# Kernel tuning notes

Measured on AMD Instinct MI355X. Metric: run time of the kernel, lower is better.

The kernel has to match this reference:

```python
import jax, jax.numpy as jnp
import numpy as np

NUM_HEADS = 16
HEAD_DIM = 64
ROPE_BASE = 160000.0


def _rope_tables(seq_len, head_dim):
    inv_freq = 1.0 / (ROPE_BASE ** (jnp.arange(0, head_dim, 2, dtype=jnp.float32) / head_dim))
    freqs = jnp.arange(seq_len, dtype=jnp.float32)[:, None] * inv_freq[None, :]  # [S, hd/2]
    return jnp.cos(freqs)[None, None], jnp.sin(freqs)[None, None]  # [1,1,S,hd/2]


def _apply_rope(x, cos, sin):
    # x: [B, nh, S, hd]; split-half rotation as in the torch module
    x1, x2 = jnp.split(x, 2, axis=-1)
    return jnp.concatenate([x1 * cos - x2 * sin, x2 * cos + x1 * sin], axis=-1)


def setup_inputs() -> dict:
    key = jax.random.key(0)
    k1, k2, k3 = jax.random.split(key, 3)
    B, S, H = 2, 2048, 1024
    hidden_states = jax.random.normal(k1, (B, S, H), dtype=jnp.float32)
    # additive causal mask: 0 for allowed, -1e9 for future positions
    causal = jnp.tril(jnp.ones((S, S), dtype=bool))
    attention_mask = jnp.where(causal, 0.0, -1e9).astype(jnp.float32)[None, None]
    Wqkv = jax.random.normal(k2, (H, 3 * H), dtype=jnp.float32) * (H ** -0.5)
    Wo = jax.random.normal(k3, (H, H), dtype=jnp.float32) * (H ** -0.5)
    return {"hidden_states": hidden_states, "attention_mask": attention_mask, "Wqkv": Wqkv, "Wo": Wo}


def reference(hidden_states, attention_mask, Wqkv, Wo):
    B, S, H = hidden_states.shape
    nh, hd = NUM_HEADS, HEAD_DIM
    scale = hd ** -0.5

    qkv = hidden_states @ Wqkv                                   # [B,S,3H]
    qkv = qkv.reshape(B, S, 3, nh, hd).transpose(2, 0, 3, 1, 4)  # [3,B,nh,S,hd]
    q, k, v = qkv[0], qkv[1], qkv[2]

    cos, sin = _rope_tables(S, hd)
    q = _apply_rope(q, cos, sin)
    k = _apply_rope(k, cos, sin)

    scores = jnp.einsum('bhqd,bhkd->bhqk', q, k) * scale + attention_mask
    attn = jax.nn.softmax(scores, axis=-1)
    out = jnp.einsum('bhqk,bhkd->bhqd', attn, v)                 # [B,nh,S,hd]
    out = out.transpose(0, 2, 1, 3).reshape(B, S, H)
    return out @ Wo
```

## Files before the change

### kernel.cpp

```cpp
#include <hip/hip_runtime.h>
#include <hip/hip_bf16.h>

typedef __bf16 bf16x8 __attribute__((ext_vector_type(8)));
typedef float f32x4 __attribute__((ext_vector_type(4)));
typedef unsigned short u16;

__device__ __forceinline__ u16 f2bf(float f) {
    union { float f; unsigned u; } x{f};
    unsigned r = x.u + 0x7fffu + ((x.u >> 16) & 1u);
    return (u16)(r >> 16);
}
__device__ __forceinline__ unsigned pk2(float a, float b) {
    union { float f; unsigned u; } x{a}, y{b};
    return ((x.u + 0x8000u) >> 16) | ((y.u + 0x8000u) & 0xffff0000u);
}
__device__ __forceinline__ float ex2(float x) { return __builtin_amdgcn_exp2f(x); }
__device__ __forceinline__ f32x4 zero4() { f32x4 z = {0.f, 0.f, 0.f, 0.f}; return z; }

__global__ void __launch_bounds__(256) prep(const float* __restrict__ hs,
                                            u16* __restrict__ Xb,
                                            const float* __restrict__ Wqkv,
                                            u16* __restrict__ Wqkvt,
                                            const float* __restrict__ Wo,
                                            u16* __restrict__ Wot,
                                            float* __restrict__ cosT,
                                            float* __restrict__ sinT) {
    __shared__ float tile[32][33];
    const int blk = blockIdx.x, t = threadIdx.x;
    if (blk < 4096) {
        int i = (blk * 256 + t) * 4;
        float4 v = *(const float4*)(hs + i);
        ushort4 o;
        o.x = f2bf(v.x); o.y = f2bf(v.y); o.z = f2bf(v.z); o.w = f2bf(v.w);
        *(ushort4*)(Xb + i) = o;
    } else if (blk < 8192) {
        const float* W; u16* Wt; int N, bx, by;
        if (blk < 7168) { int bid = blk - 4096; W = Wqkv; Wt = Wqkvt; N = 3072; bx = bid % 96; by = bid / 96; }
        else            { int bid = blk - 7168; W = Wo;   Wt = Wot;   N = 1024; bx = bid % 32; by = bid / 32; }
        const int K = 1024;
        int tx = t & 31, ty = t >> 5;
        int n0 = bx * 32, k0 = by * 32;
#pragma unroll
        for (int i = 0; i < 32; i += 8)
            tile[ty + i][tx] = W[(size_t)(k0 + ty + i) * N + n0 + tx];
        __syncthreads();
#pragma unroll
        for (int i = 0; i < 32; i += 8)
            Wt[(size_t)(n0 + ty + i) * K + k0 + tx] = f2bf(tile[tx][ty + i]);
    } else {
        int idx = (blk - 8192) * 256 + t;
        int d = idx & 31, s = idx >> 5;
        float inv = expf(-(float)d * 0.374466538f);
        float th = (float)s * inv;
        cosT[idx] = cosf(th);
        sinT[idx] = sinf(th);
    }
}

struct GemmCtx {
    f32x4 acc[4][4];
    int m16, q4, wm, wn;
};
template <int KDIM>
__device__ __forceinline__ void gemm_loop(const u16* __restrict__ A,
                                          const u16* __restrict__ Bt,
                                          int bm, int bn, GemmCtx& cx,
                                          u16 (*As)[128][40], u16 (*Bs)[128][40]) {
    const int t = threadIdx.x;
    const int lane = t & 63, w = t >> 6;
    cx.wm = w >> 1; cx.wn = w & 1;
    cx.m16 = lane & 15; cx.q4 = lane >> 4;
    const int r = t >> 1, c0 = (t & 1) * 16;

    const u16* Ag = A + (size_t)(bm * 128 + r) * KDIM + c0;
    const u16* Bg = Bt + (size_t)(bn * 128 + r) * KDIM + c0;

#pragma unroll
    for (int i = 0; i < 4; i++)
#pragma unroll
        for (int j = 0; j < 4; j++) cx.acc[i][j] = zero4();

    uint4 a0 = *(const uint4*)(Ag);
    uint4 a1 = *(const uint4*)(Ag + 8);
    uint4 b0 = *(const uint4*)(Bg);
    uint4 b1 = *(const uint4*)(Bg + 8);

    for (int k0 = 0; k0 < KDIM; k0 += 32) {
        const int bi = (k0 >> 5) & 1;
        *(uint4*)&As[bi][r][c0] = a0; *(uint4*)&As[bi][r][c0 + 8] = a1;
        *(uint4*)&Bs[bi][r][c0] = b0; *(uint4*)&Bs[bi][r][c0 + 8] = b1;
        if (k0 + 32 < KDIM) {
            a0 = *(const uint4*)(Ag + k0 + 32);
            a1 = *(const uint4*)(Ag + k0 + 40);
            b0 = *(const uint4*)(Bg + k0 + 32);
            b1 = *(const uint4*)(Bg + k0 + 40);
        }
        __syncthreads();
        bf16x8 af[4], bf[4];
#pragma unroll
        for (int i = 0; i < 4; i++)
            af[i] = *(const bf16x8*)&As[bi][cx.wm * 64 + i * 16 + cx.m16][cx.q4 * 8];
#pragma unroll
        for (int j = 0; j < 4; j++)
            bf[j] = *(const bf16x8*)&Bs[bi][cx.wn * 64 + j * 16 + cx.m16][cx.q4 * 8];
#pragma unroll
        for (int i = 0; i < 4; i++)
#pragma unroll
            for (int j = 0; j < 4; j++)
                cx.acc[i][j] = __builtin_amdgcn_mfma_f32_16x16x32_bf16(af[i], bf[j], cx.acc[i][j], 0, 0, 0);
    }
}

__global__ void __launch_bounds__(256) gemm_qkv(const u16* __restrict__ A,
                                                const u16* __restrict__ Bt,
                                                const float* __restrict__ cosT,
                                                const float* __restrict__ sinT,
                                                u16* __restrict__ Q,
                                                u16* __restrict__ Kd,
                                                u16* __restrict__ Vt) {
    __shared__ __align__(16) u16 As[2][128][40];
    __shared__ __align__(16) u16 Bs[2][128][40];
    GemmCtx cx;
    const int bm = blockIdx.y, bn = blockIdx.x;
    gemm_loop<1024>(A, Bt, bm, bn, cx, As, Bs);
    const int m16 = cx.m16, q4 = cx.q4;

    const int colbase = bn * 128 + cx.wn * 64;
    const int type = colbase >> 10;
    const int h = (colbase & 1023) >> 6;
    const int rbase = bm * 128 + cx.wm * 64;

    if (type == 2) {
#pragma unroll
        for (int i = 0; i < 4; i++) {
            int s0 = rbase + i * 16 + q4 * 4;
            int b = s0 >> 11, sl = s0 & 2047;
            size_t ob = (size_t)(b * 16 + h) * 64 * 2048;
#pragma unroll
            for (int j = 0; j < 4; j++) {
                int d = j * 16 + m16;
                ushort4 o;
                o.x = f2bf(cx.acc[i][j][0]);
                o.y = f2bf(cx.acc[i][j][1]);
                o.z = f2bf(cx.acc[i][j][2]);
                o.w = f2bf(cx.acc[i][j][3]);
                *(ushort4*)&Vt[ob + (size_t)d * 2048 + sl] = o;
            }
        }
    } else {
        u16* dst = (type == 0) ? Q : Kd;
        const float qs = (type == 0) ? 0.1803368801f  : 1.0f;
#pragma unroll
        for (int i = 0; i < 4; i++)
#pragma unroll
            for (int rr = 0; rr < 4; rr++) {
                int r = rbase + i * 16 + q4 * 4 + rr;
                int b = r >> 11, s = r & 2047;
                size_t ob = ((size_t)((b * 16 + h) * 2048 + s)) * 64;
#pragma unroll
                for (int j2 = 0; j2 < 2; j2++) {
                    int d = j2 * 16 + m16;
                    float cs = cosT[s * 32 + d];
                    float sn = sinT[s * 32 + d];
                    float x1 = cx.acc[i][j2][rr];
                    float x2 = cx.acc[i][j2 + 2][rr];
                    dst[ob + d]      = f2bf((x1 * cs - x2 * sn) * qs);
                    dst[ob + d + 32] = f2bf((x2 * cs + x1 * sn) * qs);
                }
            }
    }
}

__global__ void __launch_bounds__(256) gemm_out(const u16* __restrict__ A,
                                                const u16* __restrict__ Bt,
                                                float* __restrict__ C) {
    __shared__ __align__(16) u16 As[2][128][40];
    __shared__ __align__(16) u16 Bs[2][128][40];
    GemmCtx cx;
    const int bm = blockIdx.y, bn = blockIdx.x;
    gemm_loop<1024>(A, Bt, bm, bn, cx, As, Bs);
    const int N = 1024;
#pragma unroll
    for (int i = 0; i < 4; i++)
#pragma unroll
        for (int j = 0; j < 4; j++)
#pragma unroll
            for (int rr = 0; rr < 4; rr++) {
                int row = bm * 128 + cx.wm * 64 + i * 16 + cx.q4 * 4 + rr;
                int col = bn * 128 + cx.wn * 64 + j * 16 + cx.m16;
                C[(size_t)row * N + col] = cx.acc[i][j][rr];
            }
}

__global__ void __launch_bounds__(256) attn_kernel(const u16* __restrict__ Q,
                                                   const u16* __restrict__ Kg_,
                                                   const u16* __restrict__ Vtg_,
                                                   u16* __restrict__ O) {
    __shared__ __align__(16) u16 Ks[2][64][72];
    __shared__ __align__(16) u16 Vt[2][64][72];
    __shared__ __align__(16) u16 Pt[4][16][72];
    const int t = threadIdx.x, w = t >> 6;
    const int m16 = t & 15, q4 = (t & 63) >> 4;
    const int bx = blockIdx.x, bh = blockIdx.y;
    const size_t base = (size_t)bh * 2048 * 64;
    const int b = bh >> 4, h = bh & 15;
    const int skey = t >> 2, sc = (t & 3) * 16;

#pragma unroll 1
    for (int ph = 0; ph < 2; ph++) {
        const int qt = ph ? (31 - bx) : bx;
        const int qrow = qt * 64 + w * 16 + m16;
        const u16* Qg = Q + base + (size_t)qrow * 64;
        bf16x8 qf0 = *(const bf16x8*)(Qg + q4 * 8);
        bf16x8 qf1 = *(const bf16x8*)(Qg + 32 + q4 * 8);

        f32x4 occ[4];
#pragma unroll
        for (int dc = 0; dc < 4; dc++) occ[dc] = zero4();
        float li = 0.f;

        const u16* Kb0 = Kg_ + base + skey * 64 + sc;
        const u16* Vt0 = Vtg_ + base + (size_t)skey * 2048 + sc;
        uint4 ka = *(const uint4*)(Kb0);
        uint4 kb = *(const uint4*)(Kb0 + 8);
        uint4 va = *(const uint4*)(Vt0);
        uint4 vb = *(const uint4*)(Vt0 + 8);

#pragma unroll 1
        for (int jt = 0; jt <= qt; jt++) {
            const int bi = jt & 1;
            *(uint4*)&Ks[bi][skey][sc] = ka;
            *(uint4*)&Ks[bi][skey][sc + 8] = kb;
            *(uint4*)&Vt[bi][skey][sc] = va;
            *(uint4*)&Vt[bi][skey][sc + 8] = vb;
            if (jt < qt) {
                const u16* Kn = Kb0 + (size_t)(jt + 1) * 4096;
                const u16* Vn = Vt0 + (size_t)(jt + 1) * 64;
                ka = *(const uint4*)(Kn);
                kb = *(const uint4*)(Kn + 8);
                va = *(const uint4*)(Vn);
                vb = *(const uint4*)(Vn + 8);
            }
            __syncthreads();

            f32x4 st[4];
#pragma unroll
            for (int c = 0; c < 4; c++) st[c] = zero4();
#pragma unroll
            for (int c = 0; c < 4; c++) {
                bf16x8 kf0 = *(const bf16x8*)&Ks[bi][c * 16 + m16][q4 * 8];
                bf16x8 kf1 = *(const bf16x8*)&Ks[bi][c * 16 + m16][32 + q4 * 8];
                st[c] = __builtin_amdgcn_mfma_f32_16x16x32_bf16(kf0, qf0, st[c], 0, 0, 0);
                st[c] = __builtin_amdgcn_mfma_f32_16x16x32_bf16(kf1, qf1, st[c], 0, 0, 0);
            }

            float pv[4][4];
#pragma unroll
            for (int c = 0; c < 4; c++)
#pragma unroll
                for (int rr = 0; rr < 4; rr++) pv[c][rr] = st[c][rr];
            if (jt == qt) {
                const int ql = w * 16 + m16;
#pragma unroll
                for (int c = 0; c < 4; c++)
#pragma unroll
                    for (int rr = 0; rr < 4; rr++)
                        if (c * 16 + q4 * 4 + rr > ql) pv[c][rr] = -1e30f;
            }

#pragma unroll
            for (int c = 0; c < 4; c++) {
                float p0 = ex2(pv[c][0] - 24.f);
                float p1 = ex2(pv[c][1] - 24.f);
                float p2 = ex2(pv[c][2] - 24.f);
                float p3 = ex2(pv[c][3] - 24.f);
                li += (p0 + p1) + (p2 + p3);
                uint2 pkd = make_uint2(pk2(p0, p1), pk2(p2, p3));
                *(uint2*)&Pt[w][m16][c * 16 + q4 * 4] = pkd;
            }

#pragma unroll
            for (int ks = 0; ks < 2; ks++) {
                bf16x8 pf = *(const bf16x8*)&Pt[w][m16][ks * 32 + q4 * 8];
#pragma unroll
                for (int dc = 0; dc < 4; dc++) {
                    bf16x8 vf = *(const bf16x8*)&Vt[bi][dc * 16 + m16][ks * 32 + q4 * 8];
                    occ[dc] = __builtin_amdgcn_mfma_f32_16x16x32_bf16(vf, pf, occ[dc], 0, 0, 0);
                }
            }
        }

        li += __shfl_xor(li, 16);
        li += __shfl_xor(li, 32);
        float rli = 1.0f / li;
        u16* Op = O + ((size_t)(b * 2048 + qrow)) * 1024 + h * 64 + q4 * 4;
#pragma unroll
        for (int dc = 0; dc < 4; dc++) {
            ushort4 o;
            o.x = f2bf(occ[dc][0] * rli);
            o.y = f2bf(occ[dc][1] * rli);
            o.z = f2bf(occ[dc][2] * rli);
            o.w = f2bf(occ[dc][3] * rli);
            *(ushort4*)(Op + dc * 16) = o;
        }
        __syncthreads();
    }
}

extern "C" void kernel_launch(void* const* d_in, const int* in_sizes, int n_in,
                              void* d_out, int out_size, void* d_ws, size_t ws_size,
                              hipStream_t stream) {
    const float* hs   = (const float*)d_in[0];
    const float* Wqkv = (const float*)d_in[2];
    const float* Wo   = (const float*)d_in[3];
    float* out = (float*)d_out;

    const int BS = 4096;
    const int H = 1024, N3 = 3072;
    const int SH = 32 * 2048 * 64;

    u16* Xb    = (u16*)d_ws;
    u16* Wqkvt = Xb + (size_t)BS * H;
    u16* Wot   = Wqkvt + (size_t)N3 * H;
    u16* Qb    = Wot + (size_t)H * H;
    u16* Kb    = Qb + SH;
    u16* Vtb   = Kb + SH;
    u16* AOb   = Vtb + SH;
    float* cosT = (float*)(AOb + (size_t)BS * H);
    float* sinT = cosT + 2048 * 32;

    prep<<<8448, 256, 0, stream>>>(hs, Xb, Wqkv, Wqkvt, Wo, Wot, cosT, sinT);

    gemm_qkv<<<dim3(N3 / 128, BS / 128), 256, 0, stream>>>(Xb, Wqkvt, cosT, sinT,
                                                           Qb, Kb, Vtb);

    attn_kernel<<<dim3(16, 32), 256, 0, stream>>>(Qb, Kb, Vtb, AOb);

    gemm_out<<<dim3(H / 128, BS / 128), 256, 0, stream>>>(AOb, Wot, out);
}
```

Baseline: 201.1 us.

## Load GEMM A operand straight to registers; attention handles two query tiles per block

In the shared GEMM loop, each wave now loads its A fragments directly from global memory into registers, prefetched one k-step ahead. Only B is staged through shared memory, and the k loop is fully unrolled. This removes the A LDS writes and reads but doubles global reads of A, since both column-waves fetch the same rows. The attention kernel drops the balanced pairing of query tiles bx and 31-bx. Each block now processes two adjacent 64-row query tiles that share every K/V tile load from LDS, which halves K/V staging per query row but makes work per block uneven across the grid.

```diff
diff --git a/kernel.cpp b/kernel.cpp
--- a/kernel.cpp
+++ b/kernel.cpp
@@ -65,41 +65,45 @@
 __device__ __forceinline__ void gemm_loop(const u16* __restrict__ A,
                                           const u16* __restrict__ Bt,
                                           int bm, int bn, GemmCtx& cx,
-                                          u16 (*As)[128][40], u16 (*Bs)[128][40]) {
+                                          u16 (*Bs)[128][40]) {
     const int t = threadIdx.x;
     const int lane = t & 63, w = t >> 6;
     cx.wm = w >> 1; cx.wn = w & 1;
     cx.m16 = lane & 15; cx.q4 = lane >> 4;
     const int r = t >> 1, c0 = (t & 1) * 16;
 
-    const u16* Ag = A + (size_t)(bm * 128 + r) * KDIM + c0;
     const u16* Bg = Bt + (size_t)(bn * 128 + r) * KDIM + c0;
+    const u16* Ag = A + (size_t)(bm * 128 + cx.wm * 64 + cx.m16) * KDIM + cx.q4 * 8;
 
 #pragma unroll
     for (int i = 0; i < 4; i++)
 #pragma unroll
         for (int j = 0; j < 4; j++) cx.acc[i][j] = zero4();
 
-    uint4 a0 = *(const uint4*)(Ag);
-    uint4 a1 = *(const uint4*)(Ag + 8);
     uint4 b0 = *(const uint4*)(Bg);
     uint4 b1 = *(const uint4*)(Bg + 8);
-
+    bf16x8 afn[4];
+#pragma unroll
+    for (int i = 0; i < 4; i++)
+        afn[i] = *(const bf16x8*)(Ag + (size_t)i * 16 * KDIM);
+
+#pragma unroll
     for (int k0 = 0; k0 < KDIM; k0 += 32) {
         const int bi = (k0 >> 5) & 1;
-        *(uint4*)&As[bi][r][c0] = a0; *(uint4*)&As[bi][r][c0 + 8] = a1;
-        *(uint4*)&Bs[bi][r][c0] = b0; *(uint4*)&Bs[bi][r][c0 + 8] = b1;
+        *(uint4*)&Bs[bi][r][c0] = b0;
+        *(uint4*)&Bs[bi][r][c0 + 8] = b1;
+        bf16x8 af[4];
+#pragma unroll
+        for (int i = 0; i < 4; i++) af[i] = afn[i];
         if (k0 + 32 < KDIM) {
-            a0 = *(const uint4*)(Ag + k0 + 32);
-            a1 = *(const uint4*)(Ag + k0 + 40);
             b0 = *(const uint4*)(Bg + k0 + 32);
             b1 = *(const uint4*)(Bg + k0 + 40);
+#pragma unroll
+            for (int i = 0; i < 4; i++)
+                afn[i] = *(const bf16x8*)(Ag + k0 + 32 + (size_t)i * 16 * KDIM);
         }
         __syncthreads();
-        bf16x8 af[4], bf[4];
-#pragma unroll
-        for (int i = 0; i < 4; i++)
-            af[i] = *(const bf16x8*)&As[bi][cx.wm * 64 + i * 16 + cx.m16][cx.q4 * 8];
+        bf16x8 bf[4];
 #pragma unroll
         for (int j = 0; j < 4; j++)
             bf[j] = *(const bf16x8*)&Bs[bi][cx.wn * 64 + j * 16 + cx.m16][cx.q4 * 8];
@@ -118,11 +122,10 @@
                                                 u16* __restrict__ Q,
                                                 u16* __restrict__ Kd,
                                                 u16* __restrict__ Vt) {
-    __shared__ __align__(16) u16 As[2][128][40];
     __shared__ __align__(16) u16 Bs[2][128][40];
     GemmCtx cx;
     const int bm = blockIdx.y, bn = blockIdx.x;
-    gemm_loop<1024>(A, Bt, bm, bn, cx, As, Bs);
+    gemm_loop<1024>(A, Bt, bm, bn, cx, Bs);
     const int m16 = cx.m16, q4 = cx.q4;
 
     const int colbase = bn * 128 + cx.wn * 64;
@@ -174,11 +177,10 @@
 __global__ void __launch_bounds__(256) gemm_out(const u16* __restrict__ A,
                                                 const u16* __restrict__ Bt,
                                                 float* __restrict__ C) {
-    __shared__ __align__(16) u16 As[2][128][40];
     __shared__ __align__(16) u16 Bs[2][128][40];
     GemmCtx cx;
     const int bm = blockIdx.y, bn = blockIdx.x;
-    gemm_loop<1024>(A, Bt, bm, bn, cx, As, Bs);
+    gemm_loop<1024>(A, Bt, bm, bn, cx, Bs);
     const int N = 1024;
 #pragma unroll
     for (int i = 0; i < 4; i++)
@@ -198,7 +200,7 @@
                                                    u16* __restrict__ O) {
     __shared__ __align__(16) u16 Ks[2][64][72];
     __shared__ __align__(16) u16 Vt[2][64][72];
-    __shared__ __align__(16) u16 Pt[4][16][72];
+    __shared__ __align__(16) u16 Pt[4][2][16][72];
     const int t = threadIdx.x, w = t >> 6;
     const int m16 = t & 15, q4 = (t & 63) >> 4;
     const int bx = blockIdx.x, bh = blockIdx.y;
@@ -206,60 +208,69 @@
     const int b = bh >> 4, h = bh & 15;
     const int skey = t >> 2, sc = (t & 3) * 16;
 
+    const int jg0 = 2 * bx;
+    const int jtmax = 2 * bx + 1;
+
+    const int qrow0 = bx * 128 + w * 16 + m16;
+    const u16* Qg = Q + base + (size_t)qrow0 * 64;
+    bf16x8 qa0 = *(const bf16x8*)(Qg + q4 * 8);
+    bf16x8 qa1 = *(const bf16x8*)(Qg + 32 + q4 * 8);
+    bf16x8 qb0 = *(const bf16x8*)(Qg + 64 * 64 + q4 * 8);
+    bf16x8 qb1 = *(const bf16x8*)(Qg + 64 * 64 + 32 + q4 * 8);
+
+    f32x4 occ0[4], occ1[4];
+#pragma unroll
+    for (int dc = 0; dc < 4; dc++) { occ0[dc] = zero4(); occ1[dc] = zero4(); }
+    float li0 = 0.f, li1 = 0.f;
+
+    const u16* Kb0 = Kg_ + base + skey * 64 + sc;
+    const u16* Vt0 = Vtg_ + base + (size_t)skey * 2048 + sc;
+    uint4 ka = *(const uint4*)(Kb0);
+    uint4 kb = *(const uint4*)(Kb0 + 8);
+    uint4 va = *(const uint4*)(Vt0);
+    uint4 vb = *(const uint4*)(Vt0 + 8);
+
 #pragma unroll 1
-    for (int ph = 0; ph < 2; ph++) {
-        const int qt = ph ? (31 - bx) : bx;
-        const int qrow = qt * 64 + w * 16 + m16;
-        const u16* Qg = Q + base + (size_t)qrow * 64;
-        bf16x8 qf0 = *(const bf16x8*)(Qg + q4 * 8);
-        bf16x8 qf1 = *(const bf16x8*)(Qg + 32 + q4 * 8);
-
-        f32x4 occ[4];
-#pragma unroll
-        for (int dc = 0; dc < 4; dc++) occ[dc] = zero4();
-        float li = 0.f;
-
-        const u16* Kb0 = Kg_ + base + skey * 64 + sc;
-        const u16* Vt0 = Vtg_ + base + (size_t)skey * 2048 + sc;
-        uint4 ka = *(const uint4*)(Kb0);
-        uint4 kb = *(const uint4*)(Kb0 + 8);
-        uint4 va = *(const uint4*)(Vt0);
-        uint4 vb = *(const uint4*)(Vt0 + 8);
-
-#pragma unroll 1
-        for (int jt = 0; jt <= qt; jt++) {
-            const int bi = jt & 1;
-            *(uint4*)&Ks[bi][skey][sc] = ka;
-            *(uint4*)&Ks[bi][skey][sc + 8] = kb;
-            *(uint4*)&Vt[bi][skey][sc] = va;
-            *(uint4*)&Vt[bi][skey][sc + 8] = vb;
-            if (jt < qt) {
-                const u16* Kn = Kb0 + (size_t)(jt + 1) * 4096;
-                const u16* Vn = Vt0 + (size_t)(jt + 1) * 64;
-                ka = *(const uint4*)(Kn);
-                kb = *(const uint4*)(Kn + 8);
-                va = *(const uint4*)(Vn);
-                vb = *(const uint4*)(Vn + 8);
-            }
-            __syncthreads();
-
-            f32x4 st[4];
-#pragma unroll
-            for (int c = 0; c < 4; c++) st[c] = zero4();
-#pragma unroll
-            for (int c = 0; c < 4; c++) {
-                bf16x8 kf0 = *(const bf16x8*)&Ks[bi][c * 16 + m16][q4 * 8];
-                bf16x8 kf1 = *(const bf16x8*)&Ks[bi][c * 16 + m16][32 + q4 * 8];
-                st[c] = __builtin_amdgcn_mfma_f32_16x16x32_bf16(kf0, qf0, st[c], 0, 0, 0);
-                st[c] = __builtin_amdgcn_mfma_f32_16x16x32_bf16(kf1, qf1, st[c], 0, 0, 0);
-            }
-
+    for (int jt = 0; jt <= jtmax; jt++) {
+        const int bi = jt & 1;
+        *(uint4*)&Ks[bi][skey][sc] = ka;
+        *(uint4*)&Ks[bi][skey][sc + 8] = kb;
+        *(uint4*)&Vt[bi][skey][sc] = va;
+        *(uint4*)&Vt[bi][skey][sc + 8] = vb;
+        if (jt < jtmax) {
+            const u16* Kn = Kb0 + (size_t)(jt + 1) * 4096;
+            const u16* Vn = Vt0 + (size_t)(jt + 1) * 64;
+            ka = *(const uint4*)(Kn);
+            kb = *(const uint4*)(Kn + 8);
+            va = *(const uint4*)(Vn);
+            vb = *(const uint4*)(Vn + 8);
+        }
+        __syncthreads();
+
+        const bool g0act = (jt <= jg0);
+
+        f32x4 st0[4], st1[4];
+#pragma unroll
+        for (int c = 0; c < 4; c++) { st0[c] = zero4(); st1[c] = zero4(); }
+#pragma unroll
+        for (int c = 0; c < 4; c++) {
+            bf16x8 kf0 = *(const bf16x8*)&Ks[bi][c * 16 + m16][q4 * 8];
+            bf16x8 kf1 = *(const bf16x8*)&Ks[bi][c * 16 + m16][32 + q4 * 8];
+            if (g0act) {
+                st0[c] = __builtin_amdgcn_mfma_f32_16x16x32_bf16(kf0, qa0, st0[c], 0, 0, 0);
+                st0[c] = __builtin_amdgcn_mfma_f32_16x16x32_bf16(kf1, qa1, st0[c], 0, 0, 0);
+            }
+            st1[c] = __builtin_amdgcn_mfma_f32_16x16x32_bf16(kf0, qb0, st1[c], 0, 0, 0);
+            st1[c] = __builtin_amdgcn_mfma_f32_16x16x32_bf16(kf1, qb1, st1[c], 0, 0, 0);
+        }
+
+        if (g0act) {
             float pv[4][4];
 #pragma unroll
             for (int c = 0; c < 4; c++)
 #pragma unroll
-                for (int rr = 0; rr < 4; rr++) pv[c][rr] = st[c][rr];
-            if (jt == qt) {
+                for (int rr = 0; rr < 4; rr++) pv[c][rr] = st0[c][rr];
+            if (jt == jg0) {
                 const int ql = w * 16 + m16;
 #pragma unroll
                 for (int c = 0; c < 4; c++)
@@ -267,43 +278,75 @@
                     for (int rr = 0; rr < 4; rr++)
                         if (c * 16 + q4 * 4 + rr > ql) pv[c][rr] = -1e30f;
             }
-
 #pragma unroll
             for (int c = 0; c < 4; c++) {
                 float p0 = ex2(pv[c][0] - 24.f);
                 float p1 = ex2(pv[c][1] - 24.f);
                 float p2 = ex2(pv[c][2] - 24.f);
                 float p3 = ex2(pv[c][3] - 24.f);
-                li += (p0 + p1) + (p2 + p3);
-                uint2 pkd = make_uint2(pk2(p0, p1), pk2(p2, p3));
-                *(uint2*)&Pt[w][m16][c * 16 + q4 * 4] = pkd;
-            }
-
-#pragma unroll
-            for (int ks = 0; ks < 2; ks++) {
-                bf16x8 pf = *(const bf16x8*)&Pt[w][m16][ks * 32 + q4 * 8];
-#pragma unroll
-                for (int dc = 0; dc < 4; dc++) {
-                    bf16x8 vf = *(const bf16x8*)&Vt[bi][dc * 16 + m16][ks * 32 + q4 * 8];
-                    occ[dc] = __builtin_amdgcn_mfma_f32_16x16x32_bf16(vf, pf, occ[dc], 0, 0, 0);
-                }
-            }
-        }
-
-        li += __shfl_xor(li, 16);
-        li += __shfl_xor(li, 32);
-        float rli = 1.0f / li;
-        u16* Op = O + ((size_t)(b * 2048 + qrow)) * 1024 + h * 64 + q4 * 4;
-#pragma unroll
-        for (int dc = 0; dc < 4; dc++) {
-            ushort4 o;
-            o.x = f2bf(occ[dc][0] * rli);
-            o.y = f2bf(occ[dc][1] * rli);
-            o.z = f2bf(occ[dc][2] * rli);
-            o.w = f2bf(occ[dc][3] * rli);
-            *(ushort4*)(Op + dc * 16) = o;
-        }
-        __syncthreads();
+                li0 += (p0 + p1) + (p2 + p3);
+                *(uint2*)&Pt[w][0][m16][c * 16 + q4 * 4] = make_uint2(pk2(p0, p1), pk2(p2, p3));
+            }
+        }
+        {
+            float pv[4][4];
+#pragma unroll
+            for (int c = 0; c < 4; c++)
+#pragma unroll
+                for (int rr = 0; rr < 4; rr++) pv[c][rr] = st1[c][rr];
+            if (jt == jtmax) {
+                const int ql = w * 16 + m16;
+#pragma unroll
+                for (int c = 0; c < 4; c++)
+#pragma unroll
+                    for (int rr = 0; rr < 4; rr++)
+                        if (c * 16 + q4 * 4 + rr > ql) pv[c][rr] = -1e30f;
+            }
+#pragma unroll
+            for (int c = 0; c < 4; c++) {
+                float p0 = ex2(pv[c][0] - 24.f);
+                float p1 = ex2(pv[c][1] - 24.f);
+                float p2 = ex2(pv[c][2] - 24.f);
+                float p3 = ex2(pv[c][3] - 24.f);
+                li1 += (p0 + p1) + (p2 + p3);
+                *(uint2*)&Pt[w][1][m16][c * 16 + q4 * 4] = make_uint2(pk2(p0, p1), pk2(p2, p3));
+            }
+        }
+
+#pragma unroll
+        for (int ks = 0; ks < 2; ks++) {
+            bf16x8 pf0, pf1;
+            if (g0act) pf0 = *(const bf16x8*)&Pt[w][0][m16][ks * 32 + q4 * 8];
+            pf1 = *(const bf16x8*)&Pt[w][1][m16][ks * 32 + q4 * 8];
+#pragma unroll
+            for (int dc = 0; dc < 4; dc++) {
+                bf16x8 vf = *(const bf16x8*)&Vt[bi][dc * 16 + m16][ks * 32 + q4 * 8];
+                if (g0act)
+                    occ0[dc] = __builtin_amdgcn_mfma_f32_16x16x32_bf16(vf, pf0, occ0[dc], 0, 0, 0);
+                occ1[dc] = __builtin_amdgcn_mfma_f32_16x16x32_bf16(vf, pf1, occ1[dc], 0, 0, 0);
+            }
+        }
+    }
+
+    li0 += __shfl_xor(li0, 16); li0 += __shfl_xor(li0, 32);
+    li1 += __shfl_xor(li1, 16); li1 += __shfl_xor(li1, 32);
+    float r0 = 1.0f / li0, r1 = 1.0f / li1;
+    u16* Op0 = O + ((size_t)(b * 2048 + qrow0)) * 1024 + h * 64 + q4 * 4;
+    u16* Op1 = O + ((size_t)(b * 2048 + qrow0 + 64)) * 1024 + h * 64 + q4 * 4;
+#pragma unroll
+    for (int dc = 0; dc < 4; dc++) {
+        ushort4 o;
+        o.x = f2bf(occ0[dc][0] * r0);
+        o.y = f2bf(occ0[dc][1] * r0);
+        o.z = f2bf(occ0[dc][2] * r0);
+        o.w = f2bf(occ0[dc][3] * r0);
+        *(ushort4*)(Op0 + dc * 16) = o;
+        ushort4 p;
+        p.x = f2bf(occ1[dc][0] * r1);
+        p.y = f2bf(occ1[dc][1] * r1);
+        p.z = f2bf(occ1[dc][2] * r1);
+        p.w = f2bf(occ1[dc][3] * r1);
+        *(ushort4*)(Op1 + dc * 16) = p;
     }
 }
 
```

After: 243.7 us. +21.2%, slower.

## Use direct global-to-LDS loads in GEMMs and 128-row query tiles in attention

Applied to the files above, without the earlier changes.

The GEMM main loop now uses global_load_lds async copies into a single XOR-swizzled LDS buffer, replacing register-staged double buffering. This removes the VGPR round trip but adds a second barrier per k-step and loses prefetch overlap. The attention kernel moves to 512-thread blocks covering 128 query rows, so each K/V tile loaded into shared memory serves twice as many queries. The diagonal tile is handled by per-wave skipping and masking, and the launch grid is halved to 256 blocks, which may reduce occupancy.

```diff
diff --git a/kernel.cpp b/kernel.cpp
--- a/kernel.cpp
+++ b/kernel.cpp
@@ -16,6 +16,12 @@
 }
 __device__ __forceinline__ float ex2(float x) { return __builtin_amdgcn_exp2f(x); }
 __device__ __forceinline__ f32x4 zero4() { f32x4 z = {0.f, 0.f, 0.f, 0.f}; return z; }
+
+typedef const __attribute__((address_space(1))) unsigned int* gp1_t;
+typedef __attribute__((address_space(3))) unsigned int* lp3_t;
+__device__ __forceinline__ void async16(const u16* g, u16* l) {
+    __builtin_amdgcn_global_load_lds((gp1_t)g, (lp3_t)l, 16, 0, 0);
+}
 
 __global__ void __launch_bounds__(256) prep(const float* __restrict__ hs,
                                             u16* __restrict__ Xb,
@@ -65,44 +71,41 @@
 __device__ __forceinline__ void gemm_loop(const u16* __restrict__ A,
                                           const u16* __restrict__ Bt,
                                           int bm, int bn, GemmCtx& cx,
-                                          u16 (*As)[128][40], u16 (*Bs)[128][40]) {
+                                          u16* As, u16* Bs) {
     const int t = threadIdx.x;
     const int lane = t & 63, w = t >> 6;
     cx.wm = w >> 1; cx.wn = w & 1;
     cx.m16 = lane & 15; cx.q4 = lane >> 4;
-    const int r = t >> 1, c0 = (t & 1) * 16;
-
-    const u16* Ag = A + (size_t)(bm * 128 + r) * KDIM + c0;
-    const u16* Bg = Bt + (size_t)(bn * 128 + r) * KDIM + c0;
+
+    const int lrow = lane >> 2;
+    const int kchunk = (lane & 3) ^ ((lane >> 3) & 3);
+    const u16* Ag = A + (size_t)(bm * 128 + w * 32 + lrow) * KDIM + kchunk * 8;
+    const u16* Bg = Bt + (size_t)(bn * 128 + w * 32 + lrow) * KDIM + kchunk * 8;
+    u16* Al0 = As + (w * 32) * 32;
+    u16* Al1 = As + (w * 32 + 16) * 32;
+    u16* Bl0 = Bs + (w * 32) * 32;
+    u16* Bl1 = Bs + (w * 32 + 16) * 32;
+    const int kswz = (cx.q4 ^ ((cx.m16 >> 1) & 3)) * 8;
 
 #pragma unroll
     for (int i = 0; i < 4; i++)
 #pragma unroll
         for (int j = 0; j < 4; j++) cx.acc[i][j] = zero4();
 
-    uint4 a0 = *(const uint4*)(Ag);
-    uint4 a1 = *(const uint4*)(Ag + 8);
-    uint4 b0 = *(const uint4*)(Bg);
-    uint4 b1 = *(const uint4*)(Bg + 8);
-
     for (int k0 = 0; k0 < KDIM; k0 += 32) {
-        const int bi = (k0 >> 5) & 1;
-        *(uint4*)&As[bi][r][c0] = a0; *(uint4*)&As[bi][r][c0 + 8] = a1;
-        *(uint4*)&Bs[bi][r][c0] = b0; *(uint4*)&Bs[bi][r][c0 + 8] = b1;
-        if (k0 + 32 < KDIM) {
-            a0 = *(const uint4*)(Ag + k0 + 32);
-            a1 = *(const uint4*)(Ag + k0 + 40);
-            b0 = *(const uint4*)(Bg + k0 + 32);
-            b1 = *(const uint4*)(Bg + k0 + 40);
-        }
+        __syncthreads();
+        async16(Ag + k0, Al0);
+        async16(Ag + 16 * KDIM + k0, Al1);
+        async16(Bg + k0, Bl0);
+        async16(Bg + 16 * KDIM + k0, Bl1);
         __syncthreads();
         bf16x8 af[4], bf[4];
 #pragma unroll
         for (int i = 0; i < 4; i++)
-            af[i] = *(const bf16x8*)&As[bi][cx.wm * 64 + i * 16 + cx.m16][cx.q4 * 8];
+            af[i] = *(const bf16x8*)&As[(cx.wm * 64 + i * 16 + cx.m16) * 32 + kswz];
 #pragma unroll
         for (int j = 0; j < 4; j++)
-            bf[j] = *(const bf16x8*)&Bs[bi][cx.wn * 64 + j * 16 + cx.m16][cx.q4 * 8];
+            bf[j] = *(const bf16x8*)&Bs[(cx.wn * 64 + j * 16 + cx.m16) * 32 + kswz];
 #pragma unroll
         for (int i = 0; i < 4; i++)
 #pragma unroll
@@ -118,8 +121,8 @@
                                                 u16* __restrict__ Q,
                                                 u16* __restrict__ Kd,
                                                 u16* __restrict__ Vt) {
-    __shared__ __align__(16) u16 As[2][128][40];
-    __shared__ __align__(16) u16 Bs[2][128][40];
+    __shared__ __align__(16) u16 As[128 * 32];
+    __shared__ __align__(16) u16 Bs[128 * 32];
     GemmCtx cx;
     const int bm = blockIdx.y, bn = blockIdx.x;
     gemm_loop<1024>(A, Bt, bm, bn, cx, As, Bs);
@@ -174,8 +177,8 @@
 __global__ void __launch_bounds__(256) gemm_out(const u16* __restrict__ A,
                                                 const u16* __restrict__ Bt,
                                                 float* __restrict__ C) {
-    __shared__ __align__(16) u16 As[2][128][40];
-    __shared__ __align__(16) u16 Bs[2][128][40];
+    __shared__ __align__(16) u16 As[128 * 32];
+    __shared__ __align__(16) u16 Bs[128 * 32];
     GemmCtx cx;
     const int bm = blockIdx.y, bn = blockIdx.x;
     gemm_loop<1024>(A, Bt, bm, bn, cx, As, Bs);
@@ -192,24 +195,24 @@
             }
 }
 
-__global__ void __launch_bounds__(256) attn_kernel(const u16* __restrict__ Q,
+__global__ void __launch_bounds__(512) attn_kernel(const u16* __restrict__ Q,
                                                    const u16* __restrict__ Kg_,
                                                    const u16* __restrict__ Vtg_,
                                                    u16* __restrict__ O) {
     __shared__ __align__(16) u16 Ks[2][64][72];
-    __shared__ __align__(16) u16 Vt[2][64][72];
-    __shared__ __align__(16) u16 Pt[4][16][72];
+    __shared__ __align__(16) u16 Vs[2][64][72];
+    __shared__ __align__(16) u16 Pt[8][16][72];
     const int t = threadIdx.x, w = t >> 6;
     const int m16 = t & 15, q4 = (t & 63) >> 4;
     const int bx = blockIdx.x, bh = blockIdx.y;
     const size_t base = (size_t)bh * 2048 * 64;
     const int b = bh >> 4, h = bh & 15;
-    const int skey = t >> 2, sc = (t & 3) * 16;
+    const int skey = t >> 3, sc = (t & 7) * 8;
 
 #pragma unroll 1
     for (int ph = 0; ph < 2; ph++) {
-        const int qt = ph ? (31 - bx) : bx;
-        const int qrow = qt * 64 + w * 16 + m16;
+        const int st = ph ? (15 - bx) : bx;
+        const int qrow = st * 128 + w * 16 + m16;
         const u16* Qg = Q + base + (size_t)qrow * 64;
         bf16x8 qf0 = *(const bf16x8*)(Qg + q4 * 8);
         bf16x8 qf1 = *(const bf16x8*)(Qg + 32 + q4 * 8);
@@ -219,73 +222,69 @@
         for (int dc = 0; dc < 4; dc++) occ[dc] = zero4();
         float li = 0.f;
 
+        const int jtmax = 2 * st + 1;
+        const int jd = 2 * st + (w >> 2);
+
         const u16* Kb0 = Kg_ + base + skey * 64 + sc;
         const u16* Vt0 = Vtg_ + base + (size_t)skey * 2048 + sc;
         uint4 ka = *(const uint4*)(Kb0);
-        uint4 kb = *(const uint4*)(Kb0 + 8);
         uint4 va = *(const uint4*)(Vt0);
-        uint4 vb = *(const uint4*)(Vt0 + 8);
 
 #pragma unroll 1
-        for (int jt = 0; jt <= qt; jt++) {
+        for (int jt = 0; jt <= jtmax; jt++) {
             const int bi = jt & 1;
             *(uint4*)&Ks[bi][skey][sc] = ka;
-            *(uint4*)&Ks[bi][skey][sc + 8] = kb;
-            *(uint4*)&Vt[bi][skey][sc] = va;
-            *(uint4*)&Vt[bi][skey][sc + 8] = vb;
-            if (jt < qt) {
-                const u16* Kn = Kb0 + (size_t)(jt + 1) * 4096;
-                const u16* Vn = Vt0 + (size_t)(jt + 1) * 64;
-                ka = *(const uint4*)(Kn);
-                kb = *(const uint4*)(Kn + 8);
-                va = *(const uint4*)(Vn);
-                vb = *(const uint4*)(Vn + 8);
+            *(uint4*)&Vs[bi][skey][sc] = va;
+            if (jt < jtmax) {
+                ka = *(const uint4*)(Kb0 + (size_t)(jt + 1) * 4096);
+                va = *(const uint4*)(Vt0 + (size_t)(jt + 1) * 64);
             }
             __syncthreads();
 
-            f32x4 st[4];
-#pragma unroll
-            for (int c = 0; c < 4; c++) st[c] = zero4();
-#pragma unroll
-            for (int c = 0; c < 4; c++) {
-                bf16x8 kf0 = *(const bf16x8*)&Ks[bi][c * 16 + m16][q4 * 8];
-                bf16x8 kf1 = *(const bf16x8*)&Ks[bi][c * 16 + m16][32 + q4 * 8];
-                st[c] = __builtin_amdgcn_mfma_f32_16x16x32_bf16(kf0, qf0, st[c], 0, 0, 0);
-                st[c] = __builtin_amdgcn_mfma_f32_16x16x32_bf16(kf1, qf1, st[c], 0, 0, 0);
-            }
-
-            float pv[4][4];
-#pragma unroll
-            for (int c = 0; c < 4; c++)
-#pragma unroll
-                for (int rr = 0; rr < 4; rr++) pv[c][rr] = st[c][rr];
-            if (jt == qt) {
-                const int ql = w * 16 + m16;
+            if (jt <= jd) {
+                f32x4 stv[4];
+#pragma unroll
+                for (int c = 0; c < 4; c++) stv[c] = zero4();
+#pragma unroll
+                for (int c = 0; c < 4; c++) {
+                    bf16x8 kf0 = *(const bf16x8*)&Ks[bi][c * 16 + m16][q4 * 8];
+                    bf16x8 kf1 = *(const bf16x8*)&Ks[bi][c * 16 + m16][32 + q4 * 8];
+                    stv[c] = __builtin_amdgcn_mfma_f32_16x16x32_bf16(kf0, qf0, stv[c], 0, 0, 0);
+                    stv[c] = __builtin_amdgcn_mfma_f32_16x16x32_bf16(kf1, qf1, stv[c], 0, 0, 0);
+                }
+
+                float pv[4][4];
 #pragma unroll
                 for (int c = 0; c < 4; c++)
 #pragma unroll
-                    for (int rr = 0; rr < 4; rr++)
-                        if (c * 16 + q4 * 4 + rr > ql) pv[c][rr] = -1e30f;
-            }
-
-#pragma unroll
-            for (int c = 0; c < 4; c++) {
-                float p0 = ex2(pv[c][0] - 24.f);
-                float p1 = ex2(pv[c][1] - 24.f);
-                float p2 = ex2(pv[c][2] - 24.f);
-                float p3 = ex2(pv[c][3] - 24.f);
-                li += (p0 + p1) + (p2 + p3);
-                uint2 pkd = make_uint2(pk2(p0, p1), pk2(p2, p3));
-                *(uint2*)&Pt[w][m16][c * 16 + q4 * 4] = pkd;
-            }
-
-#pragma unroll
-            for (int ks = 0; ks < 2; ks++) {
-                bf16x8 pf = *(const bf16x8*)&Pt[w][m16][ks * 32 + q4 * 8];
-#pragma unroll
-                for (int dc = 0; dc < 4; dc++) {
-                    bf16x8 vf = *(const bf16x8*)&Vt[bi][dc * 16 + m16][ks * 32 + q4 * 8];
-                    occ[dc] = __builtin_amdgcn_mfma_f32_16x16x32_bf16(vf, pf, occ[dc], 0, 0, 0);
+                    for (int rr = 0; rr < 4; rr++) pv[c][rr] = stv[c][rr];
+                if (jt == jd) {
+                    const int ql = qrow - 64 * jt;
+#pragma unroll
+                    for (int c = 0; c < 4; c++)
+#pragma unroll
+                        for (int rr = 0; rr < 4; rr++)
+                            if (c * 16 + q4 * 4 + rr > ql) pv[c][rr] = -1e30f;
+                }
+
+#pragma unroll
+                for (int c = 0; c < 4; c++) {
+                    float p0 = ex2(pv[c][0] - 24.f);
+                    float p1 = ex2(pv[c][1] - 24.f);
+                    float p2 = ex2(pv[c][2] - 24.f);
+                    float p3 = ex2(pv[c][3] - 24.f);
+                    li += (p0 + p1) + (p2 + p3);
+                    *(uint2*)&Pt[w][m16][c * 16 + q4 * 4] = make_uint2(pk2(p0, p1), pk2(p2, p3));
+                }
+
+#pragma unroll
+                for (int ks = 0; ks < 2; ks++) {
+                    bf16x8 pf = *(const bf16x8*)&Pt[w][m16][ks * 32 + q4 * 8];
+#pragma unroll
+                    for (int dc = 0; dc < 4; dc++) {
+                        bf16x8 vf = *(const bf16x8*)&Vs[bi][dc * 16 + m16][ks * 32 + q4 * 8];
+                        occ[dc] = __builtin_amdgcn_mfma_f32_16x16x32_bf16(vf, pf, occ[dc], 0, 0, 0);
+                    }
                 }
             }
         }
@@ -334,7 +333,7 @@
     gemm_qkv<<<dim3(N3 / 128, BS / 128), 256, 0, stream>>>(Xb, Wqkvt, cosT, sinT,
                                                            Qb, Kb, Vtb);
 
-    attn_kernel<<<dim3(16, 32), 256, 0, stream>>>(Qb, Kb, Vtb, AOb);
+    attn_kernel<<<dim3(8, 32), 512, 0, stream>>>(Qb, Kb, Vtb, AOb);
 
     gemm_out<<<dim3(H / 128, BS / 128), 256, 0, stream>>>(AOb, Wot, out);
 }
```

Result: no change. 200.0 us (-0.5%).
